# Performance work log

Hardware: AMD Instinct MI355X
Metric: run time of the kernel (lower is better)

## Reference

```python
import jax, jax.numpy as jnp
import numpy as np

VOCAB = 41      # len(MOL_DICT) + 1
EMB = 512       # EMBEDDING_SIZE
HID = 1024
B, T = 128, 256


def setup_inputs() -> dict:
    key = jax.random.key(0)
    ks = jax.random.split(key, 8)
    x = jax.random.randint(ks[0], (B, T), 0, VOCAB)
    # realistic prefix padding mask: True for valid tokens, False for padding
    lengths = jax.random.randint(ks[1], (B,), T // 4, T + 1)
    padding_mask = jnp.arange(T)[None, :] < lengths[:, None]
    s = 0.05
    emb_table = jax.random.normal(ks[2], (VOCAB, EMB), jnp.float32) * s
    gru_kernel = jax.random.normal(ks[3], (EMB, 3 * HID), jnp.float32) * s
    gru_rec_kernel = jax.random.normal(ks[4], (HID, 3 * HID), jnp.float32) * s
    gru_bias = jax.random.normal(ks[5], (2, 3 * HID), jnp.float32) * s
    dense_w = jax.random.normal(ks[6], (HID, VOCAB), jnp.float32) * s
    dense_b = jnp.zeros((VOCAB,), jnp.float32)
    return {"x": x, "padding_mask": padding_mask, "emb_table": emb_table,
            "gru_kernel": gru_kernel, "gru_rec_kernel": gru_rec_kernel,
            "gru_bias": gru_bias, "dense_w": dense_w, "dense_b": dense_b}


def _gru_scan(x_proj_t, mask_t, rec_kernel, rec_bias):
    # x_proj_t: [T, B, 3H] precomputed input projections; mask_t: [T, B] bool
    def step(h, inp):
        xp, m = inp                      # xp: [B, 3H], m: [B]
        rec = h @ rec_kernel + rec_bias  # [B, 3H]  (reset_after=True)
        xz, xr, xh = jnp.split(xp, 3, axis=-1)
        rz, rr, rh = jnp.split(rec, 3, axis=-1)
        z = jax.nn.sigmoid(xz + rz)
        r = jax.nn.sigmoid(xr + rr)
        hh = jnp.tanh(xh + r * rh)
        h_new = z * h + (1.0 - z) * hh
        # masked steps carry previous state/output forward (keras semantics)
        h = jnp.where(m[:, None], h_new, h)
        return h, h

    h0 = jnp.zeros((x_proj_t.shape[1], HID), x_proj_t.dtype)
    _, outs = jax.lax.scan(step, h0, (x_proj_t, mask_t))
    return outs  # [T, B, H]


def reference(x, padding_mask, emb_table, gru_kernel, gru_rec_kernel,
              gru_bias, dense_w, dense_b):
    xe = emb_table[x]                              # [B, T, E]
    x_proj = xe @ gru_kernel + gru_bias[0]         # [B, T, 3H]
    outs = _gru_scan(jnp.transpose(x_proj, (1, 0, 2)),
                     jnp.transpose(padding_mask, (1, 0)),
                     gru_rec_kernel, gru_bias[1])  # [T, B, H]
    h = jnp.transpose(outs, (1, 0, 2))             # [B, T, H]
    logits = h @ dense_w + dense_b                 # [B, T, VOCAB]
    return logits
```

## Files before the change

kernel.cpp:

```cpp
#include <hip/hip_runtime.h>
#include <stdint.h>
#include <stddef.h>

#define VOCAB 41
#define EMB   512
#define HID   1024
#define H3    3072
#define BB    128
#define TT    256
#define BT    (BB*TT)
#define NSLOT 8
#define SLOT_U64 32768

typedef unsigned short u16;
typedef _Float16 half_t;
typedef half_t f16x8 __attribute__((ext_vector_type(8)));
typedef float f32x4 __attribute__((ext_vector_type(4)));
typedef unsigned long long u64;
typedef u64 u64x2 __attribute__((ext_vector_type(2)));

__device__ __forceinline__ float bf2f(u16 u) {
  return __uint_as_float(((uint32_t)u) << 16);
}
__device__ __forceinline__ u16 f2bf(float f) {
  uint32_t x = __float_as_uint(f);
  return (u16)((x + 0x7FFFu + ((x >> 16) & 1u)) >> 16);
}
__device__ __forceinline__ u16 f2h_bits(float f) {
  half_t h = (half_t)f;
  return __builtin_bit_cast(u16, h);
}
__device__ __forceinline__ float sigmoidf_(float x) {
  return 1.0f / (1.0f + __expf(-x));
}
__device__ __forceinline__ float tanh_fast(float x) {
  return 1.0f - 2.0f / (__expf(2.0f * x) + 1.0f);
}
__device__ __forceinline__ u64 aload64(const u64* p) {
  return __hip_atomic_load(p, __ATOMIC_RELAXED, __HIP_MEMORY_SCOPE_AGENT);
}
__device__ __forceinline__ void astore64(u64* p, u64 v) {
  __hip_atomic_store(p, v, __ATOMIC_RELAXED, __HIP_MEMORY_SCOPE_AGENT);
}
__device__ __forceinline__ void poll_flags16(const int* flc, int idx, int target) {
  int cap = 0;
  while (true) {
    int v = __hip_atomic_load(flc + idx * 16, __ATOMIC_RELAXED,
                              __HIP_MEMORY_SCOPE_AGENT);
    if (__ballot(v < target) == 0ULL) break;
    __builtin_amdgcn_s_sleep(1);
    if (++cap > (1 << 16)) break;
  }
}


__global__ void detect_kernel(const u16* __restrict__ raw, int* __restrict__ flag) {
  __shared__ int s[256];
  int tid = threadIdx.x, cnt = 0;
  for (int i = tid; i < 4096; i += 256) {
    int e = (raw[i] >> 7) & 0xFF;
    if (e >= 132) cnt++;
  }
  s[tid] = cnt; __syncthreads();
  if (tid == 0) {
    int tot = 0;
    for (int i = 0; i < 256; i++) tot += s[i];
    *flag = (tot > 4) ? 1 : 0;
  }
}

__global__ void conv_kernel(const void* __restrict__ src, float* __restrict__ dst,
                            int n, const int* __restrict__ flag) {
  int i = blockIdx.x * 256 + threadIdx.x;
  if (i >= n) return;
  if (*flag) dst[i] = ((const float*)src)[i];
  else       dst[i] = bf2f(((const u16*)src)[i]);
}

__global__ void tokm_kernel(const int* __restrict__ x,
                            const unsigned char* __restrict__ m,
                            int* __restrict__ tokm) {
  int i = blockIdx.x * 256 + threadIdx.x;
  unsigned char b0 = m[0], b1 = m[1];
  bool t;
  if (b0 == 1) {
    if (b1 != 0) t = (m[i] != 0);
    else         t = (((const int*)m)[i] != 0);
  } else if (b0 == 0x80) {
    t = (((const u16*)m)[i] != 0);
  } else {
    t = (((const float*)m)[i] != 0.0f);
  }
  tokm[i] = x[i] | (t ? 0 : 0x80000000);
}

__global__ __launch_bounds__(256) void proj_kernel(
    const void* __restrict__ emb, const void* __restrict__ gk,
    const float* __restrict__ gbf, float* __restrict__ P,
    const int* __restrict__ flag) {
  int v = blockIdx.x / (H3 / 256);
  int j = (blockIdx.x % (H3 / 256)) * 256 + threadIdx.x;
  float acc = gbf[j];
  if (*flag) {
    const float* e = (const float*)emb + v * EMB;
    const float* g = (const float*)gk;
    for (int k = 0; k < EMB; ++k) acc = fmaf(e[k], g[k * H3 + j], acc);
  } else {
    const u16* e = (const u16*)emb + v * EMB;
    const u16* g = (const u16*)gk;
    for (int k = 0; k < EMB; ++k) acc = fmaf(bf2f(e[k]), bf2f(g[k * H3 + j]), acc);
  }
  P[v * H3 + j] = acc;
}

__global__ void p2_kernel(const float* __restrict__ P, const float* __restrict__ gbf,
                          float* __restrict__ P2) {
  int gc = blockIdx.x;
  int v = threadIdx.x;
  if (v >= VOCAB) return;
  float val = P[v * H3 + gc];
  if (gc < 2048) val += gbf[H3 + gc];
  P2[gc * VOCAB + v] = val;
}

__global__ void pack_wimg_kernel(const void* __restrict__ src, u16* __restrict__ img,
                                 const int* __restrict__ flag) {
  int idx = blockIdx.x * 256 + threadIdx.x;
  int j = idx & 7;
  int t1 = idx >> 3;
  int lane = t1 & 63;
  int t2 = t1 >> 6;
  int g = t2 % 3;
  int t3 = t2 / 3;
  int ks = t3 & 31;
  int ds = t3 >> 5;
  int k = ks * 32 + (lane >> 4) * 8 + j;
  int col = g * 1024 + ds * 16 + (lane & 15);
  float val;
  if (*flag) val = ((const float*)src)[(size_t)k * H3 + col];
  else       val = bf2f(((const u16*)src)[(size_t)k * H3 + col]);
  img[idx] = f2h_bits(val);
}

__global__ void pack_dimg_kernel(const void* __restrict__ src, u16* __restrict__ img,
                                 const int* __restrict__ flag) {
  int idx = blockIdx.x * 256 + threadIdx.x;
  int j = idx & 7;
  int t1 = idx >> 3;
  int lane = t1 & 63;
  int t2 = t1 >> 6;
  int ct = t2 % 3;
  int ks = t2 / 3;
  int k = ks * 32 + (lane >> 4) * 8 + j;
  int v = ct * 16 + (lane & 15);
  float val = 0.0f;
  if (v < VOCAB) {
    if (*flag) val = ((const float*)src)[(size_t)k * VOCAB + v];
    else       val = bf2f(((const u16*)src)[(size_t)k * VOCAB + v]);
  }
  img[idx] = f2h_bits(val);
}

__global__ __launch_bounds__(256, 2) void gru_persist(
    const uint4* __restrict__ Wimg, const int* __restrict__ tokm,
    const float* __restrict__ P2, const float* __restrict__ gbf,
    u64* __restrict__ exch, u16* __restrict__ Hout,
    int* __restrict__ flags) {
  int bid = blockIdx.x;
  int gt = bid & 7, ds = bid >> 3;
  int tid = threadIdx.x;
  int w = tid >> 6, lane = tid & 63;

  __shared__ float red[4][64][13];
  __shared__ u16 tr[256];
  __shared__ float Pl[3][16][49];
  __shared__ int tokL[16 * 259];

  f16x8 breg[3][8];
  {
    const uint4* wsrc = Wimg + (size_t)ds * 96 * 64 + lane;
    #pragma unroll
    for (int k8 = 0; k8 < 8; ++k8)
      #pragma unroll
      for (int g = 0; g < 3; ++g)
        breg[g][k8] = __builtin_bit_cast(f16x8, wsrc[((w * 8 + k8) * 3 + g) * 64]);
  }

  for (int i = tid; i < 3 * 16 * VOCAB; i += 256) {
    int v = i % VOCAB;
    int t1 = i / VOCAB;
    int di = t1 & 15, g = t1 >> 4;
    Pl[g][di][v] = P2[(size_t)(g * 1024 + ds * 16 + di) * VOCAB + v];
  }
  for (int i = tid; i < 16 * 256; i += 256) {
    int rr = i >> 8, cc = i & 255;
    tokL[rr * 259 + cc] = tokm[gt * 4096 + i];
  }

  int row = tid >> 4, dim = tid & 15;
  int lane_src = (row >> 2) * 16 + dim;
  int rg = row & 3;
  float b1h = gbf[H3 + 2048 + ds * 16 + dim];
  float hcur = 0.f;
  int ks_blk = ds >> 1, q0 = (ds & 1) * 2;
  int* flc = flags + gt * 1024;
  int widx = w * 16 + (lane & 15);
  __syncthreads();

  for (int t = 0; t < TT; ++t) {
    if (t > 0) poll_flags16(flc, widx, t);

    const u64* abase = exch + (size_t)(t & 7) * SLOT_U64 + gt * 4096 +
                       (w * 8) * 128 + lane * 2;
    u64 av[16];
    #pragma unroll
    for (int i = 0; i < 8; ++i) {
      av[2 * i]     = aload64(abase + i * 128);
      av[2 * i + 1] = aload64(abase + i * 128 + 1);
    }
    f32x4 acc0 = {0.f, 0.f, 0.f, 0.f};
    f32x4 acc1 = {0.f, 0.f, 0.f, 0.f};
    f32x4 acc2 = {0.f, 0.f, 0.f, 0.f};
    #pragma unroll
    for (int k8 = 0; k8 < 8; ++k8) {
      u64x2 pair; pair.x = av[2 * k8]; pair.y = av[2 * k8 + 1];
      f16x8 a = __builtin_bit_cast(f16x8, pair);
      acc0 = __builtin_amdgcn_mfma_f32_16x16x32_f16(a, breg[0][k8], acc0, 0, 0, 0);
      acc1 = __builtin_amdgcn_mfma_f32_16x16x32_f16(a, breg[1][k8], acc1, 0, 0, 0);
      acc2 = __builtin_amdgcn_mfma_f32_16x16x32_f16(a, breg[2][k8], acc2, 0, 0, 0);
    }

    {
      float* q = red[w][lane];
      q[0] = acc0[0]; q[1] = acc0[1]; q[2]  = acc0[2]; q[3]  = acc0[3];
      q[4] = acc1[0]; q[5] = acc1[1]; q[6]  = acc1[2]; q[7]  = acc1[3];
      q[8] = acc2[0]; q[9] = acc2[1]; q[10] = acc2[2]; q[11] = acc2[3];
    }
    __syncthreads();

    {
      float a0 = 0.f, a1 = 0.f, a2 = 0.f;
      #pragma unroll
      for (int ww = 0; ww < 4; ++ww) {
        const float* q = red[ww][lane_src];
        a0 += q[rg]; a1 += q[4 + rg]; a2 += q[8 + rg];
      }
      int tm = tokL[row * 259 + t];
      int tok = tm & 0xFFFF;
      float z  = sigmoidf_(Pl[0][dim][tok] + a0);
      float r_ = sigmoidf_(Pl[1][dim][tok] + a1);
      float hh = tanh_fast(Pl[2][dim][tok] + r_ * (a2 + b1h));
      if (tm >= 0) hcur = z * hcur + (1.0f - z) * hh;
      tr[(dim >> 3) * 128 + row * 8 + (dim & 7)] = f2h_bits(hcur);
    }
    __syncthreads();

    if (w == 0) {
      u64 v = ((const u64*)tr)[lane];
      astore64(exch + (size_t)((t + 1) & 7) * SLOT_U64 + gt * 4096 +
                   ks_blk * 128 + q0 * 32 + lane, v);
      __atomic_signal_fence(__ATOMIC_SEQ_CST);
      __builtin_amdgcn_s_waitcnt(0);
      __atomic_signal_fence(__ATOMIC_SEQ_CST);
      if (lane == 0)
        __hip_atomic_fetch_add(flc + ds * 16, 1, __ATOMIC_RELAXED,
                               __HIP_MEMORY_SCOPE_AGENT);
      if (lane < 32) {
        int qq = lane >> 4, mm = lane & 15;
        uint4 hv = ((const uint4*)tr)[lane];
        int b = gt * 16 + mm;
        size_t idx = ((size_t)(b * 16 + (t >> 4)) * 32 + ks_blk) * 64 +
                     (q0 + qq) * 16 + (t & 15);
        ((uint4*)Hout)[idx] = hv;
      }
    }
  }
}

__global__ __launch_bounds__(256) void dense_mfma(
    const u16* __restrict__ HoutImg, const uint4* __restrict__ dimg,
    const float* __restrict__ dbf, void* __restrict__ out,
    const int* __restrict__ flag) {
  __shared__ uint4 Bl[48 * 64];
  int tid = threadIdx.x;
  int w = tid >> 6, lane = tid & 63;
  int quad = lane >> 4, vi = lane & 15;
  int gt0 = blockIdx.x * 8 + w * 2;

  f32x4 acc[2][3];
  #pragma unroll
  for (int i = 0; i < 2; ++i)
    #pragma unroll
    for (int c = 0; c < 3; ++c) acc[i][c] = (f32x4){0.f, 0.f, 0.f, 0.f};

  for (int half = 0; half < 2; ++half) {
    for (int i = tid; i < 48 * 64; i += 256) Bl[i] = dimg[half * 48 * 64 + i];
    __syncthreads();
    #pragma unroll
    for (int ks16 = 0; ks16 < 16; ++ks16) {
      int ks = half * 16 + ks16;
      f16x8 a0 = __builtin_bit_cast(
          f16x8, ((const uint4*)HoutImg)[((size_t)gt0 * 32 + ks) * 64 + lane]);
      f16x8 a1 = __builtin_bit_cast(
          f16x8, ((const uint4*)HoutImg)[(((size_t)gt0 + 1) * 32 + ks) * 64 + lane]);
      #pragma unroll
      for (int c = 0; c < 3; ++c) {
        f16x8 bf = __builtin_bit_cast(f16x8, Bl[(ks16 * 3 + c) * 64 + lane]);
        acc[0][c] = __builtin_amdgcn_mfma_f32_16x16x32_f16(a0, bf, acc[0][c], 0, 0, 0);
        acc[1][c] = __builtin_amdgcn_mfma_f32_16x16x32_f16(a1, bf, acc[1][c], 0, 0, 0);
      }
    }
    __syncthreads();
  }

  int isf = *flag;
  #pragma unroll
  for (int i = 0; i < 2; ++i) {
    #pragma unroll
    for (int c = 0; c < 3; ++c) {
      int v = c * 16 + vi;
      if (v >= VOCAB) continue;
      float bias = dbf[v];
      #pragma unroll
      for (int rg = 0; rg < 4; ++rg) {
        size_t bt = (size_t)(gt0 + i) * 16 + quad * 4 + rg;
        float val = acc[i][c][rg] + bias;
        if (isf) ((float*)out)[bt * VOCAB + v] = val;
        else     ((u16*)out)[bt * VOCAB + v] = f2bf(val);
      }
    }
  }
}


extern "C" void kernel_launch(void* const* d_in, const int* in_sizes, int n_in,
                              void* d_out, int out_size, void* d_ws, size_t ws_size,
                              hipStream_t stream) {
  const int* x            = (const int*)d_in[0];
  const unsigned char* mk = (const unsigned char*)d_in[1];

  char* ws = (char*)d_ws;
  int*   flag  = (int*)(ws + 0);
  float* dbf   = (float*)(ws + 4 * 1024);
  float* gbf   = (float*)(ws + 8 * 1024);
  int*   flags = (int*)(ws + 32 * 1024);
  int*   tokm  = (int*)(ws + 64 * 1024);
  u16*   dimg  = (u16*)(ws + 192 * 1024);
  float* P     = (float*)(ws + 288 * 1024);
  float* P2    = (float*)(ws + 800 * 1024);
  u64*   exch  = (u64*)(ws + 1312 * 1024);
  u16*   Wimg  = (u16*)(ws + 3456 * 1024);
  u16*   Hout  = (u16*)(ws + 10 * 1024 * 1024);

  detect_kernel<<<1, 256, 0, stream>>>((const u16*)d_in[4], flag);
  conv_kernel<<<(2 * H3 + 255) / 256, 256, 0, stream>>>(d_in[5], gbf, 2 * H3, flag);
  conv_kernel<<<1, 256, 0, stream>>>(d_in[7], dbf, VOCAB, flag);
  tokm_kernel<<<BT / 256, 256, 0, stream>>>(x, mk, tokm);
  proj_kernel<<<VOCAB * (H3 / 256), 256, 0, stream>>>(d_in[2], d_in[3], gbf, P, flag);
  p2_kernel<<<H3, 64, 0, stream>>>(P, gbf, P2);
  pack_wimg_kernel<<<(64 * 32 * 3 * 64 * 8) / 256, 256, 0, stream>>>(d_in[4], Wimg, flag);
  pack_dimg_kernel<<<(32 * 3 * 64 * 8) / 256, 256, 0, stream>>>(d_in[6], dimg, flag);
  hipMemsetAsync(flags, 0, 32 * 1024, stream);
  hipMemsetAsync(exch, 0, SLOT_U64 * 8, stream);

  gru_persist<<<512, 256, 0, stream>>>((const uint4*)Wimg, tokm, P2, gbf,
                                       exch, Hout, flags);
  dense_mfma<<<256, 256, 0, stream>>>(Hout, (const uint4*)dimg, dbf, d_out, flag);
}
```

Measured before the change: 1.204 ms.

## Halve GRU persistent grid: each block owns 32 hidden dims instead of 16

The persistent GRU kernel now runs 256 blocks instead of 512, with each block holding recurrent weights for 32 hidden columns per gate (6 MFMA B-fragments in registers). This halves the number of producers each group polls per step and the number of flag atomics. Each block does twice the MFMA and gate work per timestep and needs roughly twice the weight registers, with launch bounds relaxed to one block per SM. The weight packing, exchange layout, flags sizing and Hout write pattern are adjusted to match.

```diff
diff --git a/kernel.cpp b/kernel.cpp
--- a/kernel.cpp
+++ b/kernel.cpp
@@ -42,7 +42,7 @@
 __device__ __forceinline__ void astore64(u64* p, u64 v) {
   __hip_atomic_store(p, v, __ATOMIC_RELAXED, __HIP_MEMORY_SCOPE_AGENT);
 }
-__device__ __forceinline__ void poll_flags16(const int* flc, int idx, int target) {
+__device__ __forceinline__ void poll_flags8(const int* flc, int idx, int target) {
   int cap = 0;
   while (true) {
     int v = __hip_atomic_load(flc + idx * 16, __ATOMIC_RELAXED,
@@ -130,12 +130,13 @@
   int t1 = idx >> 3;
   int lane = t1 & 63;
   int t2 = t1 >> 6;
-  int g = t2 % 3;
-  int t3 = t2 / 3;
+  int c = t2 % 6;
+  int t3 = t2 / 6;
   int ks = t3 & 31;
   int ds = t3 >> 5;
+  int g = c >> 1, dh = c & 1;
   int k = ks * 32 + (lane >> 4) * 8 + j;
-  int col = g * 1024 + ds * 16 + (lane & 15);
+  int col = g * 1024 + ds * 32 + dh * 16 + (lane & 15);
   float val;
   if (*flag) val = ((const float*)src)[(size_t)k * H3 + col];
   else       val = bf2f(((const u16*)src)[(size_t)k * H3 + col]);
@@ -161,7 +162,7 @@
   img[idx] = f2h_bits(val);
 }
 
-__global__ __launch_bounds__(256, 2) void gru_persist(
+__global__ __launch_bounds__(256, 1) void gru_persist(
     const uint4* __restrict__ Wimg, const int* __restrict__ tokm,
     const float* __restrict__ P2, const float* __restrict__ gbf,
     u64* __restrict__ exch, u16* __restrict__ Hout,
@@ -171,44 +172,44 @@
   int tid = threadIdx.x;
   int w = tid >> 6, lane = tid & 63;
 
-  __shared__ float red[4][64][13];
-  __shared__ u16 tr[256];
-  __shared__ float Pl[3][16][49];
+  __shared__ float red[4][64][25];
+  __shared__ u16 tr[512];
+  __shared__ float Pl[3][32][41];
   __shared__ int tokL[16 * 259];
 
-  f16x8 breg[3][8];
+  f16x8 breg[6][8];
   {
-    const uint4* wsrc = Wimg + (size_t)ds * 96 * 64 + lane;
+    const uint4* wsrc = Wimg + (size_t)ds * (32 * 6) * 64 + lane;
     #pragma unroll
     for (int k8 = 0; k8 < 8; ++k8)
       #pragma unroll
-      for (int g = 0; g < 3; ++g)
-        breg[g][k8] = __builtin_bit_cast(f16x8, wsrc[((w * 8 + k8) * 3 + g) * 64]);
-  }
-
-  for (int i = tid; i < 3 * 16 * VOCAB; i += 256) {
+      for (int c = 0; c < 6; ++c)
+        breg[c][k8] = __builtin_bit_cast(f16x8, wsrc[((w * 8 + k8) * 6 + c) * 64]);
+  }
+
+  for (int i = tid; i < 3 * 32 * VOCAB; i += 256) {
     int v = i % VOCAB;
     int t1 = i / VOCAB;
-    int di = t1 & 15, g = t1 >> 4;
-    Pl[g][di][v] = P2[(size_t)(g * 1024 + ds * 16 + di) * VOCAB + v];
+    int di = t1 & 31, g = t1 >> 5;
+    Pl[g][di][v] = P2[(size_t)(g * 1024 + ds * 32 + di) * VOCAB + v];
   }
   for (int i = tid; i < 16 * 256; i += 256) {
     int rr = i >> 8, cc = i & 255;
     tokL[rr * 259 + cc] = tokm[gt * 4096 + i];
   }
 
-  int row = tid >> 4, dim = tid & 15;
-  int lane_src = (row >> 2) * 16 + dim;
+  int row = tid >> 4, dimb = tid & 15;
+  int lane_src = (row >> 2) * 16 + dimb;
   int rg = row & 3;
-  float b1h = gbf[H3 + 2048 + ds * 16 + dim];
-  float hcur = 0.f;
-  int ks_blk = ds >> 1, q0 = (ds & 1) * 2;
-  int* flc = flags + gt * 1024;
-  int widx = w * 16 + (lane & 15);
+  float b1h0 = gbf[H3 + 2048 + ds * 32 + dimb];
+  float b1h1 = gbf[H3 + 2048 + ds * 32 + dimb + 16];
+  float hc0 = 0.f, hc1 = 0.f;
+  int* flc = flags + gt * 512;
+  int widx = w * 8 + (lane & 7);
   __syncthreads();
 
   for (int t = 0; t < TT; ++t) {
-    if (t > 0) poll_flags16(flc, widx, t);
+    if (t > 0) poll_flags8(flc, widx, t);
 
     const u64* abase = exch + (size_t)(t & 7) * SLOT_U64 + gt * 4096 +
                        (w * 8) * 128 + lane * 2;
@@ -218,59 +219,72 @@
       av[2 * i]     = aload64(abase + i * 128);
       av[2 * i + 1] = aload64(abase + i * 128 + 1);
     }
-    f32x4 acc0 = {0.f, 0.f, 0.f, 0.f};
-    f32x4 acc1 = {0.f, 0.f, 0.f, 0.f};
-    f32x4 acc2 = {0.f, 0.f, 0.f, 0.f};
+    f32x4 acc[6];
+    #pragma unroll
+    for (int c = 0; c < 6; ++c) acc[c] = (f32x4){0.f, 0.f, 0.f, 0.f};
     #pragma unroll
     for (int k8 = 0; k8 < 8; ++k8) {
       u64x2 pair; pair.x = av[2 * k8]; pair.y = av[2 * k8 + 1];
       f16x8 a = __builtin_bit_cast(f16x8, pair);
-      acc0 = __builtin_amdgcn_mfma_f32_16x16x32_f16(a, breg[0][k8], acc0, 0, 0, 0);
-      acc1 = __builtin_amdgcn_mfma_f32_16x16x32_f16(a, breg[1][k8], acc1, 0, 0, 0);
-      acc2 = __builtin_amdgcn_mfma_f32_16x16x32_f16(a, breg[2][k8], acc2, 0, 0, 0);
+      #pragma unroll
+      for (int c = 0; c < 6; ++c)
+        acc[c] = __builtin_amdgcn_mfma_f32_16x16x32_f16(a, breg[c][k8], acc[c], 0, 0, 0);
     }
 
     {
       float* q = red[w][lane];
-      q[0] = acc0[0]; q[1] = acc0[1]; q[2]  = acc0[2]; q[3]  = acc0[3];
-      q[4] = acc1[0]; q[5] = acc1[1]; q[6]  = acc1[2]; q[7]  = acc1[3];
-      q[8] = acc2[0]; q[9] = acc2[1]; q[10] = acc2[2]; q[11] = acc2[3];
+      #pragma unroll
+      for (int c = 0; c < 6; ++c)
+        #pragma unroll
+        for (int r = 0; r < 4; ++r) q[c * 4 + r] = acc[c][r];
     }
     __syncthreads();
 
     {
-      float a0 = 0.f, a1 = 0.f, a2 = 0.f;
-      #pragma unroll
-      for (int ww = 0; ww < 4; ++ww) {
-        const float* q = red[ww][lane_src];
-        a0 += q[rg]; a1 += q[4 + rg]; a2 += q[8 + rg];
-      }
       int tm = tokL[row * 259 + t];
       int tok = tm & 0xFFFF;
-      float z  = sigmoidf_(Pl[0][dim][tok] + a0);
-      float r_ = sigmoidf_(Pl[1][dim][tok] + a1);
-      float hh = tanh_fast(Pl[2][dim][tok] + r_ * (a2 + b1h));
-      if (tm >= 0) hcur = z * hcur + (1.0f - z) * hh;
-      tr[(dim >> 3) * 128 + row * 8 + (dim & 7)] = f2h_bits(hcur);
+      #pragma unroll
+      for (int dh = 0; dh < 2; ++dh) {
+        float a0 = 0.f, a1 = 0.f, a2 = 0.f;
+        #pragma unroll
+        for (int ww = 0; ww < 4; ++ww) {
+          const float* q = red[ww][lane_src];
+          a0 += q[(0 * 2 + dh) * 4 + rg];
+          a1 += q[(1 * 2 + dh) * 4 + rg];
+          a2 += q[(2 * 2 + dh) * 4 + rg];
+        }
+        int dglob = dimb + dh * 16;
+        float z  = sigmoidf_(Pl[0][dglob][tok] + a0);
+        float r_ = sigmoidf_(Pl[1][dglob][tok] + a1);
+        float b1h = dh ? b1h1 : b1h0;
+        float hh = tanh_fast(Pl[2][dglob][tok] + r_ * (a2 + b1h));
+        float h = dh ? hc1 : hc0;
+        if (tm >= 0) h = z * h + (1.0f - z) * hh;
+        if (dh) hc1 = h; else hc0 = h;
+        tr[(dglob >> 3) * 128 + row * 8 + (dglob & 7)] = f2h_bits(h);
+      }
     }
     __syncthreads();
 
     if (w == 0) {
-      u64 v = ((const u64*)tr)[lane];
-      astore64(exch + (size_t)((t + 1) & 7) * SLOT_U64 + gt * 4096 +
-                   ks_blk * 128 + q0 * 32 + lane, v);
+      u64 v0 = ((const u64*)tr)[lane];
+      u64 v1 = ((const u64*)tr)[lane + 64];
+      u64* ebase = exch + (size_t)((t + 1) & 7) * SLOT_U64 + gt * 4096 +
+                   ds * 128;
+      astore64(ebase + lane, v0);
+      astore64(ebase + 64 + lane, v1);
       __atomic_signal_fence(__ATOMIC_SEQ_CST);
       __builtin_amdgcn_s_waitcnt(0);
       __atomic_signal_fence(__ATOMIC_SEQ_CST);
       if (lane == 0)
         __hip_atomic_fetch_add(flc + ds * 16, 1, __ATOMIC_RELAXED,
                                __HIP_MEMORY_SCOPE_AGENT);
-      if (lane < 32) {
-        int qq = lane >> 4, mm = lane & 15;
+      {
+        int quad = lane >> 4, mm = lane & 15;
         uint4 hv = ((const uint4*)tr)[lane];
         int b = gt * 16 + mm;
-        size_t idx = ((size_t)(b * 16 + (t >> 4)) * 32 + ks_blk) * 64 +
-                     (q0 + qq) * 16 + (t & 15);
+        size_t idx = ((size_t)(b * 16 + (t >> 4)) * 32 + ds) * 64 +
+                     quad * 16 + (t & 15);
         ((uint4*)Hout)[idx] = hv;
       }
     }
@@ -358,12 +372,12 @@
   tokm_kernel<<<BT / 256, 256, 0, stream>>>(x, mk, tokm);
   proj_kernel<<<VOCAB * (H3 / 256), 256, 0, stream>>>(d_in[2], d_in[3], gbf, P, flag);
   p2_kernel<<<H3, 64, 0, stream>>>(P, gbf, P2);
-  pack_wimg_kernel<<<(64 * 32 * 3 * 64 * 8) / 256, 256, 0, stream>>>(d_in[4], Wimg, flag);
+  pack_wimg_kernel<<<(32 * 32 * 6 * 64 * 8) / 256, 256, 0, stream>>>(d_in[4], Wimg, flag);
   pack_dimg_kernel<<<(32 * 3 * 64 * 8) / 256, 256, 0, stream>>>(d_in[6], dimg, flag);
-  hipMemsetAsync(flags, 0, 32 * 1024, stream);
+  hipMemsetAsync(flags, 0, 16 * 1024, stream);
   hipMemsetAsync(exch, 0, SLOT_U64 * 8, stream);
 
-  gru_persist<<<512, 256, 0, stream>>>((const uint4*)Wimg, tokm, P2, gbf,
+  gru_persist<<<256, 256, 0, stream>>>((const uint4*)Wimg, tokm, P2, gbf,
                                        exch, Hout, flags);
   dense_mfma<<<256, 256, 0, stream>>>(Hout, (const uint4*)dimg, dbf, d_out, flag);
 }
```

After: 995.7 us. -17.3%, faster.
